# Performance work log

Hardware: AMD Instinct MI355X
Metric: run time of the kernel (lower is better)

The kernel has to match this reference:

```python
import jax, jax.numpy as jnp
import numpy as np


def _lstm_last(x, w_ih, w_hh, b_ih, b_hh):
    # x: [M, T, D] -> last hidden state [M, H]; PyTorch gate order i,f,g,o
    M = x.shape[0]
    H = w_hh.shape[1]
    xi = jnp.einsum('mtd,gd->tmg', x, w_ih) + b_ih + b_hh  # [T, M, 4H]
    def step(carry, xt):
        h, c = carry
        gates = xt + h @ w_hh.T
        i, f, g, o = jnp.split(gates, 4, axis=-1)
        c = jax.nn.sigmoid(f) * c + jax.nn.sigmoid(i) * jnp.tanh(g)
        h = jax.nn.sigmoid(o) * jnp.tanh(c)
        return (h, c), None
    z = jnp.zeros((M, H), x.dtype)
    (h, _), _ = jax.lax.scan(step, (z, z), xi)
    return h


def _gcn_conv(x, edge_index, w, b):
    # Symmetric-normalized GCN conv with self loops (PyG GCNConv defaults).
    # x: [BT, N, F] -> [BT, N, Hg]
    N = x.shape[1]
    loops = jnp.arange(N, dtype=edge_index.dtype)
    src = jnp.concatenate([edge_index[0], loops])
    dst = jnp.concatenate([edge_index[1], loops])
    deg = jnp.zeros((N,), x.dtype).at[dst].add(jnp.ones((), x.dtype))
    dinv = jax.lax.rsqrt(deg)  # deg >= 1 thanks to self loops
    norm = (dinv[src] * dinv[dst])[:, None]  # [E+N, 1]
    xw = x @ w                               # [BT, N, Hg]
    msg = xw[:, src, :] * norm               # gather along node axis
    out = jnp.zeros_like(xw).at[:, dst, :].add(msg)  # scatter-add
    return out + b


def setup_inputs() -> dict:
    key = jax.random.key(0)
    ks = jax.random.split(key, 16)
    B, T, N, F = 2, 12, 10000, 16
    Hg, H, P, E = 32, 64, 4, 160000
    sc = 0.1
    return {
        'era5_seq': jax.random.normal(ks[0], (B, T, N, F), jnp.float32),
        'zeta_seq': jax.random.normal(ks[1], (B, T, N), jnp.float32),
        'edge_index': jax.random.randint(ks[2], (2, E), 0, N, jnp.int32),
        'gcn_w': jax.random.normal(ks[3], (F, Hg), jnp.float32) * sc,
        'gcn_b': jnp.zeros((Hg,), jnp.float32),
        'w_ih1': jax.random.normal(ks[4], (4 * H, Hg), jnp.float32) * sc,
        'w_hh1': jax.random.normal(ks[5], (4 * H, H), jnp.float32) * sc,
        'b_ih1': jax.random.normal(ks[6], (4 * H,), jnp.float32) * sc,
        'b_hh1': jax.random.normal(ks[7], (4 * H,), jnp.float32) * sc,
        'w_ih2': jax.random.normal(ks[8], (4 * H, 1), jnp.float32) * sc,
        'w_hh2': jax.random.normal(ks[9], (4 * H, H), jnp.float32) * sc,
        'b_ih2': jax.random.normal(ks[10], (4 * H,), jnp.float32) * sc,
        'b_hh2': jax.random.normal(ks[11], (4 * H,), jnp.float32) * sc,
        'fc_w': jax.random.normal(ks[12], (P, 2 * H), jnp.float32) * sc,
        'fc_b': jnp.zeros((P,), jnp.float32),
    }


def reference(era5_seq, zeta_seq, edge_index, gcn_w, gcn_b, w_ih1, w_hh1, b_ih1, b_hh1, w_ih2, w_hh2, b_ih2, b_hh2, fc_w, fc_b):
    B, T, N, F = era5_seq.shape
    Hg = gcn_w.shape[1]
    # GCN over all (b, t) slices at once (replaces nested python loops)
    h = _gcn_conv(era5_seq.reshape(B * T, N, F), edge_index, gcn_w, gcn_b)
    gcn_seq = h.reshape(B, T, N, Hg).transpose(0, 2, 1, 3).reshape(B * N, T, Hg)
    spatial_feat = _lstm_last(gcn_seq, w_ih1, w_hh1, b_ih1, b_hh1)  # [B*N, H]
    z_seq = zeta_seq.transpose(0, 2, 1).reshape(B * N, T, 1)
    zeta_feat = _lstm_last(z_seq, w_ih2, w_hh2, b_ih2, b_hh2)        # [B*N, H]
    combined = jnp.concatenate([spatial_feat, zeta_feat], axis=-1)
    y = combined @ fc_w.T + fc_b                                     # [B*N, P]
    return y.reshape(B, N, -1).transpose(0, 2, 1)                    # [B, P, N]
```

## Files before the change

### kernel.cpp

```cpp
#include <hip/hip_runtime.h>
#include <hip/hip_bf16.h>
#include <stdint.h>

#define NN 10000
#define EE 160000
#define BB 2
#define TT 12
#define FF 16
#define HG 32
#define HH 64
#define PP 4
#define BT (BB*TT)
#define MM (BB*NN)
#define CAP 96
#define L2E 1.4426950408889634f

typedef _Float16 half8 __attribute__((ext_vector_type(8)));
typedef _Float16 h2 __attribute__((ext_vector_type(2)));
typedef float f32x4 __attribute__((ext_vector_type(4)));

union UP { uint32_t u; h2 h; };
union H8U { uint32_t u[4]; half8 v; };

__device__ __forceinline__ float sigm2(float a) {
  return __builtin_amdgcn_rcpf(1.0f + __builtin_amdgcn_exp2f(-a));
}
__device__ __forceinline__ float tanh2(float a) {
  return fmaf(-2.0f, __builtin_amdgcn_rcpf(1.0f + __builtin_amdgcn_exp2f(a)), 1.0f);
}
__device__ __forceinline__ float tanh2g(float a) {
  return fmaf(-2.0f * (2.0f * L2E),
              __builtin_amdgcn_rcpf(1.0f + __builtin_amdgcn_exp2f(a)),
              2.0f * L2E);
}

__device__ __forceinline__ void barrier_lds() {
  asm volatile("s_waitcnt lgkmcnt(0)" ::: "memory");
  __builtin_amdgcn_s_barrier();
  asm volatile("" ::: "memory");
}

#define FILL_BLKS (EE / 256)
#define PREP_BLKS ((NN * BT * 8) / 256)
__global__ __launch_bounds__(256) void k_prepfill(
    const int* __restrict__ eidx, int* __restrict__ cnt, int* __restrict__ csr,
    const float* __restrict__ era5, uint32_t* __restrict__ xt,
    const float* __restrict__ w_ih1, const float* __restrict__ w_hh1,
    const float* __restrict__ b_ih1, const float* __restrict__ b_hh1,
    const float* __restrict__ w_ih2, const float* __restrict__ w_hh2,
    const float* __restrict__ b_ih2, const float* __restrict__ b_hh2,
    uint32_t* __restrict__ wbuf) {
  const int bid = blockIdx.x;
  const int tid = threadIdx.x;
  if (bid < FILL_BLKS) {
    int e = bid * 256 + tid;
    int d = eidx[EE + e];
    int pos = atomicAdd(&cnt[d], 1);
    if (pos < CAP) csr[d * CAP + pos] = eidx[e];
    return;
  }
  if (bid < FILL_BLKS + PREP_BLKS) {
    int D = (bid - FILL_BLKS) * 256 + tid;
    int f2 = D & 7;
    int bt = (D >> 3) % BT;
    int n = D / (8 * BT);
    const float* src = era5 + ((size_t)bt * NN + n) * FF + f2 * 2;
    UP u; u.h[0] = (_Float16)src[0]; u.h[1] = (_Float16)src[1];
    xt[D] = u.u;
    return;
  }
  const int wave = tid >> 6;
  const int lane = tid & 63;
  const int col = lane & 15;
  const int quad = lane >> 4;
#pragma unroll
  for (int g = 0; g < 4; ++g) {
    const float sc = (g == 2) ? 2.0f * L2E : L2E;
    int ncol = 16 * (wave + 4 * g) + col;
    wbuf[(0 + g) * 256 + tid] = __float_as_uint((b_ih1[ncol] + b_hh1[ncol]) * sc);
    wbuf[(4 + g) * 256 + tid] = __float_as_uint((b_ih2[ncol] + b_hh2[ncol]) * sc);
    wbuf[(8 + g) * 256 + tid] = __float_as_uint(w_ih2[ncol] * sc);
    H8U bx;
#pragma unroll
    for (int j = 0; j < 8; ++j)
      bx.v[j] = (_Float16)(w_ih1[ncol * HG + quad * 8 + j] * sc);
#pragma unroll
    for (int d = 0; d < 4; ++d) wbuf[(12 + g * 4 + d) * 256 + tid] = bx.u[d];
#pragma unroll
    for (int c2 = 0; c2 < 2; ++c2) {
      H8U b1, b2;
#pragma unroll
      for (int j = 0; j < 8; ++j) {
        b1.v[j] = (_Float16)(w_hh1[ncol * HH + c2 * 32 + quad * 8 + j] * sc);
        b2.v[j] = (_Float16)(w_hh2[ncol * HH + c2 * 32 + quad * 8 + j] * sc);
      }
#pragma unroll
      for (int d = 0; d < 4; ++d) {
        wbuf[(28 + (g * 2 + c2) * 4 + d) * 256 + tid] = b1.u[d];
        wbuf[(60 + (g * 2 + c2) * 4 + d) * 256 + tid] = b2.u[d];
      }
    }
  }
}

__global__ __launch_bounds__(256) void k_gather(const uint32_t* __restrict__ xt,
                                                const int* __restrict__ csr,
                                                const int* __restrict__ cnt,
                                                const float* __restrict__ gw,
                                                const float* __restrict__ gb,
                                                uint32_t* __restrict__ gout) {
  __shared__ float wsm[FF * HG];
  __shared__ float gbs[HG];
  __shared__ float agg[4][BT][FF];
  const int tid = threadIdx.x;
  wsm[tid] = gw[tid];
  wsm[tid + 256] = gw[tid + 256];
  if (tid < HG) gbs[tid] = gb[tid];

  const int dloc = tid >> 6, lane = tid & 63;
  const int dst = blockIdx.x * 4 + dloc;
  const int cdst = min(cnt[dst], CAP);
  const float dinv_d = rsqrtf((float)cdst + 1.0f);

  float acc[6];
#pragma unroll
  for (int i = 0; i < 6; ++i) acc[i] = 0.f;

  for (int base = 0; base < cdst; base += 64) {
    int mine = base + lane;
    int sv = dst; float dvv = 0.f;
    if (mine < cdst) {
      sv = csr[dst * CAP + mine];
      dvv = rsqrtf((float)cnt[sv] + 1.0f);
    }
    const int lim = min(64, cdst - base);
    for (int j = 0; j < lim; j += 4) {
      int sj[4]; float dj[4];
#pragma unroll
      for (int u = 0; u < 4; ++u) {
        int idx = j + u;
        sj[u] = __shfl(sv, idx);
        float d = __shfl(dvv, idx);
        dj[u] = (idx < lim) ? d : 0.f;
      }
      uint32_t dw[4][3];
#pragma unroll
      for (int u = 0; u < 4; ++u) {
        const uint32_t* row = xt + (size_t)sj[u] * 192;
#pragma unroll
        for (int k = 0; k < 3; ++k) dw[u][k] = row[lane + 64 * k];
      }
#pragma unroll
      for (int u = 0; u < 4; ++u) {
#pragma unroll
        for (int k = 0; k < 3; ++k) {
          UP up; up.u = dw[u][k];
          acc[2 * k]     = fmaf((float)up.h[0], dj[u], acc[2 * k]);
          acc[2 * k + 1] = fmaf((float)up.h[1], dj[u], acc[2 * k + 1]);
        }
      }
    }
  }
  const uint32_t* srow = xt + (size_t)dst * 192;
#pragma unroll
  for (int k = 0; k < 3; ++k) {
    UP u; u.u = srow[lane + 64 * k];
    int d0 = lane + 64 * k;
    int bt = d0 >> 3, f = (d0 & 7) * 2;
    agg[dloc][bt][f]     = (acc[2 * k]     + (float)u.h[0] * dinv_d) * dinv_d;
    agg[dloc][bt][f + 1] = (acc[2 * k + 1] + (float)u.h[1] * dinv_d) * dinv_d;
  }
  __syncthreads();
#pragma unroll
  for (int k = 0; k < 3; ++k) {
    int d0 = lane + 64 * k;
    int t = d0 >> 4, c0 = (d0 & 15) * 2;
#pragma unroll
    for (int b = 0; b < 2; ++b) {
      const float* av = agg[dloc][b * TT + t];
      float v0 = gbs[c0], v1 = gbs[c0 + 1];
#pragma unroll
      for (int f = 0; f < FF; ++f) {
        v0 = fmaf(av[f], wsm[f * HG + c0], v0);
        v1 = fmaf(av[f], wsm[f * HG + c0 + 1], v1);
      }
      UP u; u.h[0] = (_Float16)v0; u.h[1] = (_Float16)v1;
      gout[((size_t)(b * NN + dst)) * 192 + d0] = u.u;
    }
  }
}

__global__ __launch_bounds__(256) void k_lstmfc(
    const _Float16* __restrict__ gout, const float* __restrict__ zeta,
    const uint32_t* __restrict__ wbuf,
    const float* __restrict__ fc_w, const float* __restrict__ fc_b,
    float* __restrict__ out) {
  const int m0 = blockIdx.x * 16;
  const int b = (m0 >= NN) ? 1 : 0;
  const int n0 = m0 - b * NN;
  const int tid = threadIdx.x;
  const int wave = tid >> 6;
  const int lane = tid & 63;
  const int col = lane & 15;
  const int quad = lane >> 4;

  float bias1[4], bias2[4], wx[4];
  H8U Bx[4], Bh1[4][2], Bh2[4][2];
#pragma unroll
  for (int g = 0; g < 4; ++g) {
    bias1[g] = __uint_as_float(wbuf[(0 + g) * 256 + tid]);
    bias2[g] = __uint_as_float(wbuf[(4 + g) * 256 + tid]);
    wx[g]    = __uint_as_float(wbuf[(8 + g) * 256 + tid]);
#pragma unroll
    for (int d = 0; d < 4; ++d) Bx[g].u[d] = wbuf[(12 + g * 4 + d) * 256 + tid];
#pragma unroll
    for (int c2 = 0; c2 < 2; ++c2)
#pragma unroll
      for (int d = 0; d < 4; ++d) {
        Bh1[g][c2].u[d] = wbuf[(28 + (g * 2 + c2) * 4 + d) * 256 + tid];
        Bh2[g][c2].u[d] = wbuf[(60 + (g * 2 + c2) * 4 + d) * 256 + tid];
      }
  }
  f32x4 bv1[4];
#pragma unroll
  for (int g = 0; g < 4; ++g) {
    f32x4 v = {bias1[g], bias1[g], bias1[g], bias1[g]};
    bv1[g] = v;
  }

  __shared__ float zbuf[TT][16];
  if (tid < TT * 16) {
    int t = tid >> 4, s = tid & 15;
    zbuf[t][s] = zeta[((size_t)b * TT + t) * NN + n0 + s];
  }
  __shared__ __align__(16) _Float16 hb1[2][16 * 72];
  __shared__ __align__(16) _Float16 hb2[2][16 * 72];
  __shared__ float fcb[16][132];

  const _Float16* gbase = gout + (size_t)(m0 + col) * (TT * HG) + quad * 8;
  half8 A0 = *(const half8*)(gbase);

  float c1[4] = {0.f, 0.f, 0.f, 0.f}, c2v[4] = {0.f, 0.f, 0.f, 0.f};
  float h1f[4], h2f[4];

  barrier_lds();

#pragma unroll
  for (int t = 0; t < TT; ++t) {
    const int p = t & 1;
    if (t > 0) {
#pragma unroll
      for (int r = 0; r < 4; ++r) {
        int a = (quad * 4 + r) * 72 + 16 * wave + col;
        hb1[p][a] = (_Float16)h1f[r];
        hb2[p][a] = (_Float16)h2f[r];
      }
    }
    f32x4 a1[4], a2[4];
    const f32x4 z4 = *(const f32x4*)(&zbuf[t][quad * 4]);
#pragma unroll
    for (int g = 0; g < 4; ++g) {
      a1[g] = __builtin_amdgcn_mfma_f32_16x16x32_f16(A0, Bx[g].v, bv1[g], 0, 0, 0);
#pragma unroll
      for (int r = 0; r < 4; ++r)
        a2[g][r] = fmaf(wx[g], z4[r], bias2[g]);
    }
    if (t < TT - 1) A0 = *(const half8*)(gbase + (t + 1) * HG);
    if (t > 0) {
      barrier_lds();
      const half8 A11 = *(const half8*)(&hb1[p][col * 72 + quad * 8]);
      const half8 A21 = *(const half8*)(&hb1[p][col * 72 + 32 + quad * 8]);
      const half8 A12 = *(const half8*)(&hb2[p][col * 72 + quad * 8]);
      const half8 A22 = *(const half8*)(&hb2[p][col * 72 + 32 + quad * 8]);
#pragma unroll
      for (int g = 0; g < 4; ++g) {
        a1[g] = __builtin_amdgcn_mfma_f32_16x16x32_f16(A11, Bh1[g][0].v, a1[g], 0, 0, 0);
        a1[g] = __builtin_amdgcn_mfma_f32_16x16x32_f16(A21, Bh1[g][1].v, a1[g], 0, 0, 0);
        a2[g] = __builtin_amdgcn_mfma_f32_16x16x32_f16(A12, Bh2[g][0].v, a2[g], 0, 0, 0);
        a2[g] = __builtin_amdgcn_mfma_f32_16x16x32_f16(A22, Bh2[g][1].v, a2[g], 0, 0, 0);
      }
    }
#pragma unroll
    for (int r = 0; r < 4; ++r) {
      float i1 = sigm2(a1[0][r]), f1 = sigm2(a1[1][r]);
      float g1 = tanh2g(a1[2][r]), o1 = sigm2(a1[3][r]);
      c1[r] = fmaf(f1, c1[r], i1 * g1);
      h1f[r] = o1 * tanh2(c1[r]);
      float i2 = sigm2(a2[0][r]), f2 = sigm2(a2[1][r]);
      float g2 = tanh2g(a2[2][r]), o2 = sigm2(a2[3][r]);
      c2v[r] = fmaf(f2, c2v[r], i2 * g2);
      h2f[r] = o2 * tanh2(c2v[r]);
    }
  }
#pragma unroll
  for (int r = 0; r < 4; ++r) {
    fcb[quad * 4 + r][16 * wave + col] = h1f[r];
    fcb[quad * 4 + r][64 + 16 * wave + col] = h2f[r];
  }
  barrier_lds();
  if (tid < 64) {
    int pp = tid >> 4, s = tid & 15;
    const f32x4* wr = (const f32x4*)(fc_w + pp * 128);
    const float* hv = fcb[s];
    float acc = fc_b[pp];
#pragma unroll
    for (int k = 0; k < 32; ++k) {
      f32x4 w4 = wr[k];
      acc += w4[0] * hv[4 * k] + w4[1] * hv[4 * k + 1] +
             w4[2] * hv[4 * k + 2] + w4[3] * hv[4 * k + 3];
    }
    out[((size_t)(b * PP + pp)) * NN + n0 + s] = acc;
  }
}

extern "C" void kernel_launch(void* const* d_in, const int* in_sizes, int n_in,
                              void* d_out, int out_size, void* d_ws, size_t ws_size,
                              hipStream_t stream) {
  (void)in_sizes; (void)n_in; (void)out_size; (void)ws_size;
  const float* era5  = (const float*)d_in[0];
  const float* zeta  = (const float*)d_in[1];
  const int*   eidx  = (const int*)d_in[2];
  const float* gcn_w = (const float*)d_in[3];
  const float* gcn_b = (const float*)d_in[4];
  const float* w_ih1 = (const float*)d_in[5];
  const float* w_hh1 = (const float*)d_in[6];
  const float* b_ih1 = (const float*)d_in[7];
  const float* b_hh1 = (const float*)d_in[8];
  const float* w_ih2 = (const float*)d_in[9];
  const float* w_hh2 = (const float*)d_in[10];
  const float* b_ih2 = (const float*)d_in[11];
  const float* b_hh2 = (const float*)d_in[12];
  const float* fc_w  = (const float*)d_in[13];
  const float* fc_b  = (const float*)d_in[14];
  float* out = (float*)d_out;

  char* ws = (char*)d_ws;
  int*      cnt  = (int*)(ws);
  int*      csr  = (int*)(ws + (64 << 10));
  uint32_t* xt   = (uint32_t*)(ws + (4ull << 20));
  uint32_t* gout = (uint32_t*)(ws + (12ull << 20));
  uint32_t* wbuf = (uint32_t*)(ws + (28ull << 20));

  hipMemsetAsync(cnt, 0, NN * sizeof(int), stream);
  k_prepfill<<<FILL_BLKS + PREP_BLKS + 1, 256, 0, stream>>>(
      eidx, cnt, csr, era5, xt,
      w_ih1, w_hh1, b_ih1, b_hh1, w_ih2, w_hh2, b_ih2, b_hh2, wbuf);
  k_gather<<<NN / 4, 256, 0, stream>>>(xt, csr, cnt, gcn_w, gcn_b, gout);
  k_lstmfc<<<MM / 16, 256, 0, stream>>>((const _Float16*)gout, zeta, wbuf,
                                        fc_w, fc_b, out);
}
```

Baseline: 175.4 us.

## Process 32 LSTM rows per block to amortize weight loads and barriers

The fused LSTM+FC kernel now handles two 16-row tiles per block instead of one, interleaving two independent MFMA recurrence chains per wave. The per-block register weight loads from wbuf and the per-step LDS barriers are amortized over twice as many rows, and the two chains give the scheduler more independent work to hide MFMA and transcendental latency. In exchange it needs more registers, which may reduce occupancy, and it halves the grid to 625 blocks. The h buffers and the FC staging buffer share a union to limit LDS growth, and rows that cross the batch boundary are handled per element.

```diff
diff --git a/kernel.cpp b/kernel.cpp
--- a/kernel.cpp
+++ b/kernel.cpp
@@ -195,9 +195,7 @@
     const uint32_t* __restrict__ wbuf,
     const float* __restrict__ fc_w, const float* __restrict__ fc_b,
     float* __restrict__ out) {
-  const int m0 = blockIdx.x * 16;
-  const int b = (m0 >= NN) ? 1 : 0;
-  const int n0 = m0 - b * NN;
+  const int m0 = blockIdx.x * 32;
   const int tid = threadIdx.x;
   const int wave = tid >> 6;
   const int lane = tid & 63;
@@ -228,20 +226,31 @@
     bv1[g] = v;
   }
 
-  __shared__ float zbuf[TT][16];
-  if (tid < TT * 16) {
-    int t = tid >> 4, s = tid & 15;
-    zbuf[t][s] = zeta[((size_t)b * TT + t) * NN + n0 + s];
-  }
-  __shared__ __align__(16) _Float16 hb1[2][16 * 72];
-  __shared__ __align__(16) _Float16 hb2[2][16 * 72];
-  __shared__ float fcb[16][132];
-
-  const _Float16* gbase = gout + (size_t)(m0 + col) * (TT * HG) + quad * 8;
-  half8 A0 = *(const half8*)(gbase);
-
-  float c1[4] = {0.f, 0.f, 0.f, 0.f}, c2v[4] = {0.f, 0.f, 0.f, 0.f};
-  float h1f[4], h2f[4];
+  __shared__ union {
+    struct {
+      __align__(16) _Float16 hb1[2][32 * 72];
+      __align__(16) _Float16 hb2[2][32 * 72];
+    } h;
+    float fcb[32][132];
+  } su;
+  __shared__ float zbuf[TT][32];
+
+  for (int i = tid; i < TT * 32; i += 256) {
+    int t = i >> 5, s = i & 31;
+    int m = m0 + s;
+    int bs = (m >= NN) ? 1 : 0;
+    int ns = m - bs * NN;
+    zbuf[t][s] = zeta[((size_t)bs * TT + t) * NN + ns];
+  }
+
+  const _Float16* gbaseA = gout + (size_t)(m0 + col) * (TT * HG) + quad * 8;
+  const _Float16* gbaseB = gbaseA + (size_t)16 * (TT * HG);
+  half8 A0A = *(const half8*)(gbaseA);
+  half8 A0B = *(const half8*)(gbaseB);
+
+  float c1A[4] = {0.f, 0.f, 0.f, 0.f}, c2A[4] = {0.f, 0.f, 0.f, 0.f};
+  float c1B[4] = {0.f, 0.f, 0.f, 0.f}, c2B[4] = {0.f, 0.f, 0.f, 0.f};
+  float h1fA[4], h2fA[4], h1fB[4], h2fB[4];
 
   barrier_lds();
 
@@ -252,56 +261,87 @@
 #pragma unroll
       for (int r = 0; r < 4; ++r) {
         int a = (quad * 4 + r) * 72 + 16 * wave + col;
-        hb1[p][a] = (_Float16)h1f[r];
-        hb2[p][a] = (_Float16)h2f[r];
-      }
-    }
-    f32x4 a1[4], a2[4];
-    const f32x4 z4 = *(const f32x4*)(&zbuf[t][quad * 4]);
+        su.h.hb1[p][a] = (_Float16)h1fA[r];
+        su.h.hb2[p][a] = (_Float16)h2fA[r];
+        su.h.hb1[p][a + 16 * 72] = (_Float16)h1fB[r];
+        su.h.hb2[p][a + 16 * 72] = (_Float16)h2fB[r];
+      }
+    }
+    f32x4 a1A[4], a2A[4], a1B[4], a2B[4];
+    const f32x4 z4A = *(const f32x4*)(&zbuf[t][quad * 4]);
+    const f32x4 z4B = *(const f32x4*)(&zbuf[t][16 + quad * 4]);
 #pragma unroll
     for (int g = 0; g < 4; ++g) {
-      a1[g] = __builtin_amdgcn_mfma_f32_16x16x32_f16(A0, Bx[g].v, bv1[g], 0, 0, 0);
-#pragma unroll
-      for (int r = 0; r < 4; ++r)
-        a2[g][r] = fmaf(wx[g], z4[r], bias2[g]);
-    }
-    if (t < TT - 1) A0 = *(const half8*)(gbase + (t + 1) * HG);
+      a1A[g] = __builtin_amdgcn_mfma_f32_16x16x32_f16(A0A, Bx[g].v, bv1[g], 0, 0, 0);
+      a1B[g] = __builtin_amdgcn_mfma_f32_16x16x32_f16(A0B, Bx[g].v, bv1[g], 0, 0, 0);
+#pragma unroll
+      for (int r = 0; r < 4; ++r) {
+        a2A[g][r] = fmaf(wx[g], z4A[r], bias2[g]);
+        a2B[g][r] = fmaf(wx[g], z4B[r], bias2[g]);
+      }
+    }
+    if (t < TT - 1) {
+      A0A = *(const half8*)(gbaseA + (t + 1) * HG);
+      A0B = *(const half8*)(gbaseB + (t + 1) * HG);
+    }
     if (t > 0) {
       barrier_lds();
-      const half8 A11 = *(const half8*)(&hb1[p][col * 72 + quad * 8]);
-      const half8 A21 = *(const half8*)(&hb1[p][col * 72 + 32 + quad * 8]);
-      const half8 A12 = *(const half8*)(&hb2[p][col * 72 + quad * 8]);
-      const half8 A22 = *(const half8*)(&hb2[p][col * 72 + 32 + quad * 8]);
+      const half8 A11A = *(const half8*)(&su.h.hb1[p][col * 72 + quad * 8]);
+      const half8 A21A = *(const half8*)(&su.h.hb1[p][col * 72 + 32 + quad * 8]);
+      const half8 A12A = *(const half8*)(&su.h.hb2[p][col * 72 + quad * 8]);
+      const half8 A22A = *(const half8*)(&su.h.hb2[p][col * 72 + 32 + quad * 8]);
+      const half8 A11B = *(const half8*)(&su.h.hb1[p][(16 + col) * 72 + quad * 8]);
+      const half8 A21B = *(const half8*)(&su.h.hb1[p][(16 + col) * 72 + 32 + quad * 8]);
+      const half8 A12B = *(const half8*)(&su.h.hb2[p][(16 + col) * 72 + quad * 8]);
+      const half8 A22B = *(const half8*)(&su.h.hb2[p][(16 + col) * 72 + 32 + quad * 8]);
 #pragma unroll
       for (int g = 0; g < 4; ++g) {
-        a1[g] = __builtin_amdgcn_mfma_f32_16x16x32_f16(A11, Bh1[g][0].v, a1[g], 0, 0, 0);
-        a1[g] = __builtin_amdgcn_mfma_f32_16x16x32_f16(A21, Bh1[g][1].v, a1[g], 0, 0, 0);
-        a2[g] = __builtin_amdgcn_mfma_f32_16x16x32_f16(A12, Bh2[g][0].v, a2[g], 0, 0, 0);
-        a2[g] = __builtin_amdgcn_mfma_f32_16x16x32_f16(A22, Bh2[g][1].v, a2[g], 0, 0, 0);
+        a1A[g] = __builtin_amdgcn_mfma_f32_16x16x32_f16(A11A, Bh1[g][0].v, a1A[g], 0, 0, 0);
+        a1A[g] = __builtin_amdgcn_mfma_f32_16x16x32_f16(A21A, Bh1[g][1].v, a1A[g], 0, 0, 0);
+        a1B[g] = __builtin_amdgcn_mfma_f32_16x16x32_f16(A11B, Bh1[g][0].v, a1B[g], 0, 0, 0);
+        a1B[g] = __builtin_amdgcn_mfma_f32_16x16x32_f16(A21B, Bh1[g][1].v, a1B[g], 0, 0, 0);
+        a2A[g] = __builtin_amdgcn_mfma_f32_16x16x32_f16(A12A, Bh2[g][0].v, a2A[g], 0, 0, 0);
+        a2A[g] = __builtin_amdgcn_mfma_f32_16x16x32_f16(A22A, Bh2[g][1].v, a2A[g], 0, 0, 0);
+        a2B[g] = __builtin_amdgcn_mfma_f32_16x16x32_f16(A12B, Bh2[g][0].v, a2B[g], 0, 0, 0);
+        a2B[g] = __builtin_amdgcn_mfma_f32_16x16x32_f16(A22B, Bh2[g][1].v, a2B[g], 0, 0, 0);
       }
     }
 #pragma unroll
     for (int r = 0; r < 4; ++r) {
-      float i1 = sigm2(a1[0][r]), f1 = sigm2(a1[1][r]);
-      float g1 = tanh2g(a1[2][r]), o1 = sigm2(a1[3][r]);
-      c1[r] = fmaf(f1, c1[r], i1 * g1);
-      h1f[r] = o1 * tanh2(c1[r]);
-      float i2 = sigm2(a2[0][r]), f2 = sigm2(a2[1][r]);
-      float g2 = tanh2g(a2[2][r]), o2 = sigm2(a2[3][r]);
-      c2v[r] = fmaf(f2, c2v[r], i2 * g2);
-      h2f[r] = o2 * tanh2(c2v[r]);
-    }
-  }
+      float i1 = sigm2(a1A[0][r]), f1 = sigm2(a1A[1][r]);
+      float g1 = tanh2g(a1A[2][r]), o1 = sigm2(a1A[3][r]);
+      c1A[r] = fmaf(f1, c1A[r], i1 * g1);
+      h1fA[r] = o1 * tanh2(c1A[r]);
+      float i2 = sigm2(a2A[0][r]), f2 = sigm2(a2A[1][r]);
+      float g2 = tanh2g(a2A[2][r]), o2 = sigm2(a2A[3][r]);
+      c2A[r] = fmaf(f2, c2A[r], i2 * g2);
+      h2fA[r] = o2 * tanh2(c2A[r]);
+      float i3 = sigm2(a1B[0][r]), f3 = sigm2(a1B[1][r]);
+      float g3 = tanh2g(a1B[2][r]), o3 = sigm2(a1B[3][r]);
+      c1B[r] = fmaf(f3, c1B[r], i3 * g3);
+      h1fB[r] = o3 * tanh2(c1B[r]);
+      float i4 = sigm2(a2B[0][r]), f4 = sigm2(a2B[1][r]);
+      float g4 = tanh2g(a2B[2][r]), o4 = sigm2(a2B[3][r]);
+      c2B[r] = fmaf(f4, c2B[r], i4 * g4);
+      h2fB[r] = o4 * tanh2(c2B[r]);
+    }
+  }
+  barrier_lds();
 #pragma unroll
   for (int r = 0; r < 4; ++r) {
-    fcb[quad * 4 + r][16 * wave + col] = h1f[r];
-    fcb[quad * 4 + r][64 + 16 * wave + col] = h2f[r];
+    su.fcb[quad * 4 + r][16 * wave + col] = h1fA[r];
+    su.fcb[quad * 4 + r][64 + 16 * wave + col] = h2fA[r];
+    su.fcb[16 + quad * 4 + r][16 * wave + col] = h1fB[r];
+    su.fcb[16 + quad * 4 + r][64 + 16 * wave + col] = h2fB[r];
   }
   barrier_lds();
-  if (tid < 64) {
-    int pp = tid >> 4, s = tid & 15;
+  if (tid < 128) {
+    int pp = tid >> 5, s = tid & 31;
+    int m = m0 + s;
+    int bs = (m >= NN) ? 1 : 0;
+    int ns = m - bs * NN;
     const f32x4* wr = (const f32x4*)(fc_w + pp * 128);
-    const float* hv = fcb[s];
+    const float* hv = su.fcb[s];
     float acc = fc_b[pp];
 #pragma unroll
     for (int k = 0; k < 32; ++k) {
@@ -309,7 +349,7 @@
       acc += w4[0] * hv[4 * k] + w4[1] * hv[4 * k + 1] +
              w4[2] * hv[4 * k + 2] + w4[3] * hv[4 * k + 3];
     }
-    out[((size_t)(b * PP + pp)) * NN + n0 + s] = acc;
+    out[((size_t)(bs * PP + pp)) * NN + ns] = acc;
   }
 }
 
@@ -346,6 +386,6 @@
       eidx, cnt, csr, era5, xt,
       w_ih1, w_hh1, b_ih1, b_hh1, w_ih2, w_hh2, b_ih2, b_hh2, wbuf);
   k_gather<<<NN / 4, 256, 0, stream>>>(xt, csr, cnt, gcn_w, gcn_b, gout);
-  k_lstmfc<<<MM / 16, 256, 0, stream>>>((const _Float16*)gout, zeta, wbuf,
+  k_lstmfc<<<MM / 32, 256, 0, stream>>>((const _Float16*)gout, zeta, wbuf,
                                         fc_w, fc_b, out);
 }
```

Result: slower. 195.1 us (+11.2%).

## Fuse GCN aggregation into LSTM kernel and fold GCN weight into input projection

Applied to the files above, without the earlier changes.

Removes the separate gather kernel and the gout intermediate. The LSTM kernel now aggregates normalized neighbor features (F=16) per node directly into shared memory. The GCN weight and bias are folded algebraically into the LSTM input weights (W_ih1·W_gcn) in the prep block, so the MFMA consumes 16-dim aggregated features zero-padded to 32. This saves one launch and the global round trip of the 32-dim GCN output. In exchange, each LSTM block pays for the irregular gather, and the per-block LDS footprint grows, which may lower occupancy.

```diff
diff --git a/kernel.cpp b/kernel.cpp
--- a/kernel.cpp
+++ b/kernel.cpp
@@ -14,6 +14,8 @@
 #define MM (BB*NN)
 #define CAP 96
 #define L2E 1.4426950408889634f
+#define XROW 96
+#define APS 648
 
 typedef _Float16 half8 __attribute__((ext_vector_type(8)));
 typedef _Float16 h2 __attribute__((ext_vector_type(2)));
@@ -41,10 +43,11 @@
 }
 
 #define FILL_BLKS (EE / 256)
-#define PREP_BLKS ((NN * BT * 8) / 256)
+#define PREP_BLKS ((MM * XROW) / 256)
 __global__ __launch_bounds__(256) void k_prepfill(
     const int* __restrict__ eidx, int* __restrict__ cnt, int* __restrict__ csr,
     const float* __restrict__ era5, uint32_t* __restrict__ xt,
+    const float* __restrict__ gcn_w, const float* __restrict__ gcn_b,
     const float* __restrict__ w_ih1, const float* __restrict__ w_hh1,
     const float* __restrict__ b_ih1, const float* __restrict__ b_hh1,
     const float* __restrict__ w_ih2, const float* __restrict__ w_hh2,
@@ -61,14 +64,24 @@
   }
   if (bid < FILL_BLKS + PREP_BLKS) {
     int D = (bid - FILL_BLKS) * 256 + tid;
-    int f2 = D & 7;
-    int bt = (D >> 3) % BT;
-    int n = D / (8 * BT);
-    const float* src = era5 + ((size_t)bt * NN + n) * FF + f2 * 2;
+    int b = D / (NN * XROW);
+    int rem = D - b * (NN * XROW);
+    int n = rem / XROW;
+    int l = rem - n * XROW;
+    int t = l >> 3, fp = l & 7;
+    const float* src = era5 + (((size_t)b * TT + t) * NN + n) * FF + fp * 2;
     UP u; u.h[0] = (_Float16)src[0]; u.h[1] = (_Float16)src[1];
     xt[D] = u.u;
     return;
   }
+  __shared__ float wl[256 * HG];
+  __shared__ float gwl[FF * HG];
+  __shared__ float gbl[HG];
+  for (int i = tid; i < 256 * HG; i += 256) wl[i] = w_ih1[i];
+  for (int i = tid; i < FF * HG; i += 256) gwl[i] = gcn_w[i];
+  if (tid < HG) gbl[tid] = gcn_b[tid];
+  __syncthreads();
+
   const int wave = tid >> 6;
   const int lane = tid & 63;
   const int col = lane & 15;
@@ -77,13 +90,22 @@
   for (int g = 0; g < 4; ++g) {
     const float sc = (g == 2) ? 2.0f * L2E : L2E;
     int ncol = 16 * (wave + 4 * g) + col;
-    wbuf[(0 + g) * 256 + tid] = __float_as_uint((b_ih1[ncol] + b_hh1[ncol]) * sc);
+    const float* wr = &wl[ncol * HG];
+    float bc = 0.f;
+    for (int hg = 0; hg < HG; ++hg) bc = fmaf(gbl[hg], wr[hg], bc);
+    wbuf[(0 + g) * 256 + tid] =
+        __float_as_uint((bc + b_ih1[ncol] + b_hh1[ncol]) * sc);
     wbuf[(4 + g) * 256 + tid] = __float_as_uint((b_ih2[ncol] + b_hh2[ncol]) * sc);
     wbuf[(8 + g) * 256 + tid] = __float_as_uint(w_ih2[ncol] * sc);
     H8U bx;
 #pragma unroll
-    for (int j = 0; j < 8; ++j)
-      bx.v[j] = (_Float16)(w_ih1[ncol * HG + quad * 8 + j] * sc);
+    for (int j = 0; j < 8; ++j) {
+      int k = quad * 8 + j;
+      float v = 0.f;
+      if (k < FF)
+        for (int hg = 0; hg < HG; ++hg) v = fmaf(gwl[k * HG + hg], wr[hg], v);
+      bx.v[j] = (_Float16)(v * sc);
+    }
 #pragma unroll
     for (int d = 0; d < 4; ++d) wbuf[(12 + g * 4 + d) * 256 + tid] = bx.u[d];
 #pragma unroll
@@ -103,95 +125,9 @@
   }
 }
 
-__global__ __launch_bounds__(256) void k_gather(const uint32_t* __restrict__ xt,
-                                                const int* __restrict__ csr,
-                                                const int* __restrict__ cnt,
-                                                const float* __restrict__ gw,
-                                                const float* __restrict__ gb,
-                                                uint32_t* __restrict__ gout) {
-  __shared__ float wsm[FF * HG];
-  __shared__ float gbs[HG];
-  __shared__ float agg[4][BT][FF];
-  const int tid = threadIdx.x;
-  wsm[tid] = gw[tid];
-  wsm[tid + 256] = gw[tid + 256];
-  if (tid < HG) gbs[tid] = gb[tid];
-
-  const int dloc = tid >> 6, lane = tid & 63;
-  const int dst = blockIdx.x * 4 + dloc;
-  const int cdst = min(cnt[dst], CAP);
-  const float dinv_d = rsqrtf((float)cdst + 1.0f);
-
-  float acc[6];
-#pragma unroll
-  for (int i = 0; i < 6; ++i) acc[i] = 0.f;
-
-  for (int base = 0; base < cdst; base += 64) {
-    int mine = base + lane;
-    int sv = dst; float dvv = 0.f;
-    if (mine < cdst) {
-      sv = csr[dst * CAP + mine];
-      dvv = rsqrtf((float)cnt[sv] + 1.0f);
-    }
-    const int lim = min(64, cdst - base);
-    for (int j = 0; j < lim; j += 4) {
-      int sj[4]; float dj[4];
-#pragma unroll
-      for (int u = 0; u < 4; ++u) {
-        int idx = j + u;
-        sj[u] = __shfl(sv, idx);
-        float d = __shfl(dvv, idx);
-        dj[u] = (idx < lim) ? d : 0.f;
-      }
-      uint32_t dw[4][3];
-#pragma unroll
-      for (int u = 0; u < 4; ++u) {
-        const uint32_t* row = xt + (size_t)sj[u] * 192;
-#pragma unroll
-        for (int k = 0; k < 3; ++k) dw[u][k] = row[lane + 64 * k];
-      }
-#pragma unroll
-      for (int u = 0; u < 4; ++u) {
-#pragma unroll
-        for (int k = 0; k < 3; ++k) {
-          UP up; up.u = dw[u][k];
-          acc[2 * k]     = fmaf((float)up.h[0], dj[u], acc[2 * k]);
-          acc[2 * k + 1] = fmaf((float)up.h[1], dj[u], acc[2 * k + 1]);
-        }
-      }
-    }
-  }
-  const uint32_t* srow = xt + (size_t)dst * 192;
-#pragma unroll
-  for (int k = 0; k < 3; ++k) {
-    UP u; u.u = srow[lane + 64 * k];
-    int d0 = lane + 64 * k;
-    int bt = d0 >> 3, f = (d0 & 7) * 2;
-    agg[dloc][bt][f]     = (acc[2 * k]     + (float)u.h[0] * dinv_d) * dinv_d;
-    agg[dloc][bt][f + 1] = (acc[2 * k + 1] + (float)u.h[1] * dinv_d) * dinv_d;
-  }
-  __syncthreads();
-#pragma unroll
-  for (int k = 0; k < 3; ++k) {
-    int d0 = lane + 64 * k;
-    int t = d0 >> 4, c0 = (d0 & 15) * 2;
-#pragma unroll
-    for (int b = 0; b < 2; ++b) {
-      const float* av = agg[dloc][b * TT + t];
-      float v0 = gbs[c0], v1 = gbs[c0 + 1];
-#pragma unroll
-      for (int f = 0; f < FF; ++f) {
-        v0 = fmaf(av[f], wsm[f * HG + c0], v0);
-        v1 = fmaf(av[f], wsm[f * HG + c0 + 1], v1);
-      }
-      UP u; u.h[0] = (_Float16)v0; u.h[1] = (_Float16)v1;
-      gout[((size_t)(b * NN + dst)) * 192 + d0] = u.u;
-    }
-  }
-}
-
 __global__ __launch_bounds__(256) void k_lstmfc(
-    const _Float16* __restrict__ gout, const float* __restrict__ zeta,
+    const uint32_t* __restrict__ xt, const int* __restrict__ csr,
+    const int* __restrict__ cnt, const float* __restrict__ zeta,
     const uint32_t* __restrict__ wbuf,
     const float* __restrict__ fc_w, const float* __restrict__ fc_b,
     float* __restrict__ out) {
@@ -204,6 +140,85 @@
   const int col = lane & 15;
   const int quad = lane >> 4;
 
+  __shared__ __align__(16) _Float16 aggf[TT * APS];
+  __shared__ union {
+    struct {
+      __align__(16) _Float16 hb1[2][16 * 72];
+      __align__(16) _Float16 hb2[2][16 * 72];
+    } h;
+    float fcb[16][132];
+  } su;
+  __shared__ float zbuf[TT][16];
+
+  {
+    uint32_t* az = (uint32_t*)aggf;
+    for (int i = tid; i < TT * APS / 2; i += 256) az[i] = 0u;
+  }
+  if (tid < TT * 16) {
+    int t = tid >> 4, s = tid & 15;
+    zbuf[t][s] = zeta[((size_t)b * TT + t) * NN + n0 + s];
+  }
+  barrier_lds();
+
+  const uint32_t* xb = xt + (size_t)b * NN * XROW;
+  const int tA = lane >> 3, fp = lane & 7;
+  const int lh = lane & 31;
+#pragma unroll
+  for (int i = 0; i < 4; ++i) {
+    const int n = n0 + wave * 4 + i;
+    const int cdst = min(cnt[n], CAP);
+    const float dinv = rsqrtf((float)cdst + 1.0f);
+    float aA0 = 0.f, aA1 = 0.f, aB0 = 0.f, aB1 = 0.f;
+    for (int base = 0; base < cdst; base += 64) {
+      int mine = base + lane;
+      int sv = n; float dvv = 0.f;
+      if (mine < cdst) {
+        sv = csr[n * CAP + mine];
+        dvv = rsqrtf((float)cnt[sv] + 1.0f);
+      }
+      const int lim = min(64, cdst - base);
+      for (int j = 0; j < lim; j += 8) {
+        int sj[8]; float dj[8];
+#pragma unroll
+        for (int u = 0; u < 8; ++u) {
+          int idx = j + u;
+          sj[u] = __shfl(sv, idx);
+          float d = __shfl(dvv, idx);
+          dj[u] = (idx < lim) ? d : 0.f;
+        }
+        uint32_t dwA[8], dwB[8];
+#pragma unroll
+        for (int u = 0; u < 8; ++u) {
+          const uint32_t* row = xb + (size_t)sj[u] * XROW;
+          dwA[u] = row[lane];
+          dwB[u] = row[64 + lh];
+        }
+#pragma unroll
+        for (int u = 0; u < 8; ++u) {
+          UP a; a.u = dwA[u];
+          aA0 = fmaf((float)a.h[0], dj[u], aA0);
+          aA1 = fmaf((float)a.h[1], dj[u], aA1);
+          UP bb; bb.u = dwB[u];
+          aB0 = fmaf((float)bb.h[0], dj[u], aB0);
+          aB1 = fmaf((float)bb.h[1], dj[u], aB1);
+        }
+      }
+    }
+    UP sA; sA.u = xb[(size_t)n * XROW + lane];
+    UP sB; sB.u = xb[(size_t)n * XROW + 64 + lh];
+    const int m = wave * 4 + i;
+    UP oA;
+    oA.h[0] = (_Float16)((aA0 + (float)sA.h[0] * dinv) * dinv);
+    oA.h[1] = (_Float16)((aA1 + (float)sA.h[1] * dinv) * dinv);
+    *(uint32_t*)&aggf[tA * APS + m * 40 + fp * 2] = oA.u;
+    if (lane < 32) {
+      UP oB;
+      oB.h[0] = (_Float16)((aB0 + (float)sB.h[0] * dinv) * dinv);
+      oB.h[1] = (_Float16)((aB1 + (float)sB.h[1] * dinv) * dinv);
+      *(uint32_t*)&aggf[(8 + (lh >> 3)) * APS + m * 40 + fp * 2] = oB.u;
+    }
+  }
+
   float bias1[4], bias2[4], wx[4];
   H8U Bx[4], Bh1[4][2], Bh2[4][2];
 #pragma unroll
@@ -228,18 +243,6 @@
     bv1[g] = v;
   }
 
-  __shared__ float zbuf[TT][16];
-  if (tid < TT * 16) {
-    int t = tid >> 4, s = tid & 15;
-    zbuf[t][s] = zeta[((size_t)b * TT + t) * NN + n0 + s];
-  }
-  __shared__ __align__(16) _Float16 hb1[2][16 * 72];
-  __shared__ __align__(16) _Float16 hb2[2][16 * 72];
-  __shared__ float fcb[16][132];
-
-  const _Float16* gbase = gout + (size_t)(m0 + col) * (TT * HG) + quad * 8;
-  half8 A0 = *(const half8*)(gbase);
-
   float c1[4] = {0.f, 0.f, 0.f, 0.f}, c2v[4] = {0.f, 0.f, 0.f, 0.f};
   float h1f[4], h2f[4];
 
@@ -252,10 +255,11 @@
 #pragma unroll
       for (int r = 0; r < 4; ++r) {
         int a = (quad * 4 + r) * 72 + 16 * wave + col;
-        hb1[p][a] = (_Float16)h1f[r];
-        hb2[p][a] = (_Float16)h2f[r];
-      }
-    }
+        su.h.hb1[p][a] = (_Float16)h1f[r];
+        su.h.hb2[p][a] = (_Float16)h2f[r];
+      }
+    }
+    const half8 A0 = *(const half8*)&aggf[t * APS + col * 40 + quad * 8];
     f32x4 a1[4], a2[4];
     const f32x4 z4 = *(const f32x4*)(&zbuf[t][quad * 4]);
 #pragma unroll
@@ -265,13 +269,12 @@
       for (int r = 0; r < 4; ++r)
         a2[g][r] = fmaf(wx[g], z4[r], bias2[g]);
     }
-    if (t < TT - 1) A0 = *(const half8*)(gbase + (t + 1) * HG);
     if (t > 0) {
       barrier_lds();
-      const half8 A11 = *(const half8*)(&hb1[p][col * 72 + quad * 8]);
-      const half8 A21 = *(const half8*)(&hb1[p][col * 72 + 32 + quad * 8]);
-      const half8 A12 = *(const half8*)(&hb2[p][col * 72 + quad * 8]);
-      const half8 A22 = *(const half8*)(&hb2[p][col * 72 + 32 + quad * 8]);
+      const half8 A11 = *(const half8*)(&su.h.hb1[p][col * 72 + quad * 8]);
+      const half8 A21 = *(const half8*)(&su.h.hb1[p][col * 72 + 32 + quad * 8]);
+      const half8 A12 = *(const half8*)(&su.h.hb2[p][col * 72 + quad * 8]);
+      const half8 A22 = *(const half8*)(&su.h.hb2[p][col * 72 + 32 + quad * 8]);
 #pragma unroll
       for (int g = 0; g < 4; ++g) {
         a1[g] = __builtin_amdgcn_mfma_f32_16x16x32_f16(A11, Bh1[g][0].v, a1[g], 0, 0, 0);
@@ -292,16 +295,17 @@
       h2f[r] = o2 * tanh2(c2v[r]);
     }
   }
+  barrier_lds();
 #pragma unroll
   for (int r = 0; r < 4; ++r) {
-    fcb[quad * 4 + r][16 * wave + col] = h1f[r];
-    fcb[quad * 4 + r][64 + 16 * wave + col] = h2f[r];
+    su.fcb[quad * 4 + r][16 * wave + col] = h1f[r];
+    su.fcb[quad * 4 + r][64 + 16 * wave + col] = h2f[r];
   }
   barrier_lds();
   if (tid < 64) {
     int pp = tid >> 4, s = tid & 15;
     const f32x4* wr = (const f32x4*)(fc_w + pp * 128);
-    const float* hv = fcb[s];
+    const float* hv = su.fcb[s];
     float acc = fc_b[pp];
 #pragma unroll
     for (int k = 0; k < 32; ++k) {
@@ -338,14 +342,12 @@
   int*      cnt  = (int*)(ws);
   int*      csr  = (int*)(ws + (64 << 10));
   uint32_t* xt   = (uint32_t*)(ws + (4ull << 20));
-  uint32_t* gout = (uint32_t*)(ws + (12ull << 20));
   uint32_t* wbuf = (uint32_t*)(ws + (28ull << 20));
 
   hipMemsetAsync(cnt, 0, NN * sizeof(int), stream);
   k_prepfill<<<FILL_BLKS + PREP_BLKS + 1, 256, 0, stream>>>(
-      eidx, cnt, csr, era5, xt,
+      eidx, cnt, csr, era5, xt, gcn_w, gcn_b,
       w_ih1, w_hh1, b_ih1, b_hh1, w_ih2, w_hh2, b_ih2, b_hh2, wbuf);
-  k_gather<<<NN / 4, 256, 0, stream>>>(xt, csr, cnt, gcn_w, gcn_b, gout);
-  k_lstmfc<<<MM / 16, 256, 0, stream>>>((const _Float16*)gout, zeta, wbuf,
+  k_lstmfc<<<MM / 16, 256, 0, stream>>>(xt, csr, cnt, zeta, wbuf,
                                         fc_w, fc_b, out);
 }
```

Result: slower. 194.7 us (+11.0%).
